# Performance work log

Measured on AMD Instinct MI355X. Metric: run time of the kernel, lower is better.

## Reference

```python
import jax, jax.numpy as jnp
import numpy as np

B, S, D, H, KD = 4, 2048, 640, 10, 64


def setup_inputs() -> dict:
    key = jax.random.key(0)
    k0, k1, k2, k3, k4 = jax.random.split(key, 5)
    x = jax.random.normal(k0, (B, S, D), dtype=jnp.float32)
    # per-head projection weights, stacked over heads: [H, D, KD]
    Wq = jax.random.normal(k1, (H, D, KD), dtype=jnp.float32) * 0.05
    Wk = jax.random.normal(k2, (H, D, KD), dtype=jnp.float32) * 0.05
    Wv = jax.random.normal(k3, (H, D, KD), dtype=jnp.float32) * 0.05
    # output projection: [H*KD, D]
    Wo = jax.random.normal(k4, (H * KD, D), dtype=jnp.float32) * 0.05
    return {"x": x, "Wq": Wq, "Wk": Wk, "Wv": Wv, "Wo": Wo}


def reference(x, Wq, Wk, Wv, Wo):
    # Batched equivalent of the per-head Python loop:
    # each head computes q=x@Wq_h, k=x@Wk_h, v=x@Wv_h, softmax(q k^T / sqrt(KD)) @ v
    q = jnp.einsum("bsd,hdk->bhsk", x, Wq)
    k = jnp.einsum("bsd,hdk->bhsk", x, Wk)
    v = jnp.einsum("bsd,hdk->bhsk", x, Wv)
    scale = 1.0 / jnp.sqrt(jnp.asarray(KD, x.dtype))
    scores = jnp.einsum("bhsk,bhtk->bhst", q, k) * scale  # [B,H,S,S]
    attn = jax.nn.softmax(scores, axis=-1)
    z = jnp.einsum("bhst,bhtk->bhsk", attn, v)  # [B,H,S,KD]
    # concat heads along last axis (head 0 first, matching the loop order)
    z = z.transpose(0, 2, 1, 3).reshape(x.shape[0], x.shape[1], H * KD)
    return jnp.einsum("bsf,fd->bsd", z, Wo)
```

## Files before the change

kernel.cpp:

```cpp
#include <hip/hip_runtime.h>
#include <hip/hip_bf16.h>

#define B_  4
#define S_  2048
#define D_  640
#define H_  10
#define KD_ 64

typedef __attribute__((ext_vector_type(8))) short  short8;
typedef __attribute__((ext_vector_type(4))) short  short4v;
typedef __attribute__((ext_vector_type(4))) float  floatx4;

static __device__ __forceinline__ short f2bf(float f) {
    union { __hip_bfloat16 h; short s; } u;
    u.h = __float2bfloat16(f);
    return u.s;
}

static __device__ __forceinline__ void gload_lds16(const void* gp, void* lp) {
    __builtin_amdgcn_global_load_lds(
        (const __attribute__((address_space(1))) unsigned int*)gp,
        (__attribute__((address_space(3))) unsigned int*)lp, 16, 0, 0);
}

__global__ __launch_bounds__(256) void pack_x(
        const float* __restrict__ x, short* __restrict__ xb) {
    int idx = (blockIdx.x * 256 + threadIdx.x) * 4;
    float4 v = *(const float4*)(x + idx);
    short4v o;
    o[0] = f2bf(v.x); o[1] = f2bf(v.y); o[2] = f2bf(v.z); o[3] = f2bf(v.w);
    *(short4v*)(xb + idx) = o;
}

__global__ __launch_bounds__(256) void transpose_w(
        const float* __restrict__ Wq, const float* __restrict__ Wk,
        const float* __restrict__ Wv, short* __restrict__ BigT) {
    __shared__ float tile[32][33];
    int m = blockIdx.z;
    int w = m / 10, h = m % 10;
    const float* W = ((w == 0) ? Wq : (w == 1) ? Wk : Wv) + h * 640 * 64;
    short* out = BigT + (w * 640 + h * 64) * 640;
    int c0 = blockIdx.x * 32;
    int r0 = blockIdx.y * 32;
    int tx = threadIdx.x & 31, ty = threadIdx.x >> 5;
    #pragma unroll
    for (int k = 0; k < 4; ++k)
        tile[ty + 8 * k][tx] = W[(r0 + ty + 8 * k) * 64 + c0 + tx];
    __syncthreads();
    #pragma unroll
    for (int k = 0; k < 4; ++k)
        out[(c0 + ty + 8 * k) * 640 + r0 + tx] = f2bf(tile[tx][ty + 8 * k]);
}

__global__ __launch_bounds__(256) void transpose_wo(
        const float* __restrict__ Wo, short* __restrict__ WoT) {
    __shared__ float tile[32][33];
    int c0 = blockIdx.x * 32;
    int r0 = blockIdx.y * 32;
    int tx = threadIdx.x & 31, ty = threadIdx.x >> 5;
    #pragma unroll
    for (int k = 0; k < 4; ++k)
        tile[ty + 8 * k][tx] = Wo[(r0 + ty + 8 * k) * 640 + c0 + tx];
    __syncthreads();
    #pragma unroll
    for (int k = 0; k < 4; ++k)
        WoT[(c0 + ty + 8 * k) * 640 + r0 + tx] = f2bf(tile[tx][ty + 8 * k]);
}

__global__ __launch_bounds__(256) void qkv_gemm(
        const short* __restrict__ X, const short* __restrict__ BigT,
        short* __restrict__ qb, short* __restrict__ kb, short* __restrict__ vtb) {
    __shared__ __align__(16) short Ab[128][64];
    __shared__ __align__(16) short Bb[128][64];

    int wave = threadIdx.x >> 6;
    int lane = threadIdx.x & 63;
    int lq = lane & 15, quad = lane >> 4;
    int wm = (wave & 1) * 64, wn = (wave >> 1) * 64;
    int tm = blockIdx.x * 128;
    int tn = blockIdx.y * 128;

    int r8 = lane >> 3;
    int sc = ((lane & 7) ^ r8) * 8;
    const short* Asrc = X    + (tm + wave * 32 + r8) * 640 + sc;
    const short* Bsrc = BigT + (tn + wave * 32 + r8) * 640 + sc;

    floatx4 acc[4][4];
    for (int a = 0; a < 4; ++a)
        for (int n = 0; n < 4; ++n)
            acc[a][n] = (floatx4){0.f, 0.f, 0.f, 0.f};

    int swz = lq & 7;
    for (int k0 = 0; k0 < 640; k0 += 64) {
        __syncthreads();
        #pragma unroll
        for (int c = 0; c < 4; ++c) {
            gload_lds16(Asrc + c * 8 * 640 + k0, &Ab[wave * 32 + c * 8][0]);
            gload_lds16(Bsrc + c * 8 * 640 + k0, &Bb[wave * 32 + c * 8][0]);
        }
        __syncthreads();

        #pragma unroll
        for (int ks = 0; ks < 2; ++ks) {
            short8 af[4], bf[4];
            #pragma unroll
            for (int t = 0; t < 4; ++t) {
                af[t] = *(const short8*)(&Ab[wm + t * 16 + lq][((ks * 4 + quad) ^ swz) * 8]);
                bf[t] = *(const short8*)(&Bb[wn + t * 16 + lq][((ks * 4 + quad) ^ swz) * 8]);
            }
            #pragma unroll
            for (int mt = 0; mt < 4; ++mt)
                #pragma unroll
                for (int nt = 0; nt < 4; ++nt)
                    acc[mt][nt] = __builtin_amdgcn_mfma_f32_16x16x32_bf16(
                        af[mt], bf[nt], acc[mt][nt], 0, 0, 0);
        }
    }

    const float qscale = 0.18033688011112042f;
    #pragma unroll
    for (int nt = 0; nt < 4; ++nt) {
        int n_base = tn + wn + nt * 16;
        int w = n_base / 640, rem = n_base % 640;
        int hh = rem / 64, kd = (rem % 64) + lq;
        #pragma unroll
        for (int mt = 0; mt < 4; ++mt) {
            #pragma unroll
            for (int r = 0; r < 4; ++r) {
                int m = tm + wm + mt * 16 + quad * 4 + r;
                int b = m >> 11, s = m & 2047;
                float val = acc[mt][nt][r];
                if (w == 0) {
                    qb[((b * H_ + hh) * S_ + s) * KD_ + kd] = f2bf(val * qscale);
                } else if (w == 1) {
                    kb[((b * H_ + hh) * S_ + s) * KD_ + kd] = f2bf(val);
                } else {
                    vtb[((b * H_ + hh) * KD_ + kd) * S_ + s] = f2bf(val);
                }
            }
        }
    }
}

__global__ __launch_bounds__(256) void attn(
        const short* __restrict__ qb, const short* __restrict__ kb,
        const short* __restrict__ vtb, short* __restrict__ zb) {
    __shared__ __align__(16) short Kbuf[2][64][64];
    __shared__ __align__(16) short Vbuf[2][64][64];
    __shared__ __align__(16) short Pbuf[4][16][72];

    int wave = threadIdx.x >> 6;
    int lane = threadIdx.x & 63;
    int lq = lane & 15, quad = lane >> 4;

    int bx = blockIdx.x;
    int xcd = bx & 7, slot = bx >> 3;
    int bh = xcd * 5 + (slot >> 5);
    int qt = slot & 31;
    int b = bh / 10, h = bh % 10;
    int q0 = qt * 64;

    const short* qp = qb + (b * H_ + h) * S_ * KD_;
    const short* kp = kb + (b * H_ + h) * S_ * KD_;
    const short* vp = vtb + (b * H_ + h) * KD_ * S_;

    int r8 = lane >> 3;
    int g  = (lane & 7) ^ r8;
    const short* kg0 = kp + (wave * 16 + r8) * 64 + g * 8;
    const short* kg1 = kp + (wave * 16 + 8 + r8) * 64 + g * 8;
    const short* vg0 = vp + (wave * 16 + r8) * (long)S_ + g * 8;
    const short* vg1 = vp + (wave * 16 + 8 + r8) * (long)S_ + g * 8;

    short8 qf0, qf1;
    {
        int row = q0 + wave * 16 + lq;
        qf0 = *(const short8*)(qp + row * 64 + quad * 8);
        qf1 = *(const short8*)(qp + row * 64 + 32 + quad * 8);
    }

    floatx4 O[4];
    for (int n = 0; n < 4; ++n) O[n] = (floatx4){0.f, 0.f, 0.f, 0.f};
    float lsum[4] = {0.f, 0.f, 0.f, 0.f};

    gload_lds16(kg0, &Kbuf[0][wave * 16][0]);
    gload_lds16(kg1, &Kbuf[0][wave * 16 + 8][0]);
    gload_lds16(vg0, &Vbuf[0][wave * 16][0]);
    gload_lds16(vg1, &Vbuf[0][wave * 16 + 8][0]);

    int p = 0;
    int sw = lq & 7;

    for (int t0 = 0; t0 < S_; t0 += 64) {
        __syncthreads();

        if (t0 + 64 < S_) {
            int pn = p ^ 1;
            gload_lds16(kg0 + (t0 + 64) * 64, &Kbuf[pn][wave * 16][0]);
            gload_lds16(kg1 + (t0 + 64) * 64, &Kbuf[pn][wave * 16 + 8][0]);
            gload_lds16(vg0 + (t0 + 64),      &Vbuf[pn][wave * 16][0]);
            gload_lds16(vg1 + (t0 + 64),      &Vbuf[pn][wave * 16 + 8][0]);
        }

        const short* Kb = &Kbuf[p][0][0];
        const short* Vb = &Vbuf[p][0][0];

        floatx4 sf[4];
        #pragma unroll
        for (int nt = 0; nt < 4; ++nt) {
            const short* krow = Kb + (nt * 16 + lq) * 64;
            short8 bk0 = *(const short8*)(krow + (quad ^ sw) * 8);
            short8 bk1 = *(const short8*)(krow + ((quad + 4) ^ sw) * 8);
            floatx4 z4 = (floatx4){0.f, 0.f, 0.f, 0.f};
            z4 = __builtin_amdgcn_mfma_f32_16x16x32_bf16(qf0, bk0, z4, 0, 0, 0);
            sf[nt] = __builtin_amdgcn_mfma_f32_16x16x32_bf16(qf1, bk1, z4, 0, 0, 0);
        }

        #pragma unroll
        for (int nt = 0; nt < 4; ++nt) {
            #pragma unroll
            for (int r = 0; r < 4; ++r) {
                float pv = __builtin_amdgcn_exp2f(sf[nt][r]);
                lsum[r] += pv;
                Pbuf[wave][quad * 4 + r][nt * 16 + lq] = f2bf(pv);
            }
        }

        #pragma unroll
        for (int ks = 0; ks < 2; ++ks) {
            short8 pf = *(const short8*)(&Pbuf[wave][lq][ks * 32 + quad * 8]);
            #pragma unroll
            for (int nt = 0; nt < 4; ++nt) {
                const short* vrow = Vb + (nt * 16 + lq) * 64;
                short8 bv = *(const short8*)(vrow + ((ks * 4 + quad) ^ sw) * 8);
                O[nt] = __builtin_amdgcn_mfma_f32_16x16x32_bf16(pf, bv, O[nt], 0, 0, 0);
            }
        }

        p ^= 1;
    }

    #pragma unroll
    for (int r = 0; r < 4; ++r) {
        float s = lsum[r];
        s += __shfl_xor(s, 1);
        s += __shfl_xor(s, 2);
        s += __shfl_xor(s, 4);
        s += __shfl_xor(s, 8);
        lsum[r] = s;
    }
    for (int nt = 0; nt < 4; ++nt) {
        for (int r = 0; r < 4; ++r) {
            int s = q0 + wave * 16 + quad * 4 + r;
            float o = O[nt][r] / lsum[r];
            zb[(b * S_ + s) * 640 + h * 64 + nt * 16 + lq] = f2bf(o);
        }
    }
}

__global__ __launch_bounds__(256) void out_gemm(
        const short* __restrict__ Z, const short* __restrict__ WoT,
        float* __restrict__ out) {
    __shared__ __align__(16) short Ab[128][64];
    __shared__ __align__(16) short Bb[128][64];

    int wave = threadIdx.x >> 6;
    int lane = threadIdx.x & 63;
    int lq = lane & 15, quad = lane >> 4;
    int wm = (wave & 1) * 64, wn = (wave >> 1) * 64;
    int tm = blockIdx.x * 128;
    int tn = blockIdx.y * 128;

    int r8 = lane >> 3;
    int sc = ((lane & 7) ^ r8) * 8;
    const short* Asrc = Z   + (tm + wave * 32 + r8) * 640 + sc;
    const short* Bsrc = WoT + (tn + wave * 32 + r8) * 640 + sc;

    floatx4 acc[4][4];
    for (int a = 0; a < 4; ++a)
        for (int n = 0; n < 4; ++n)
            acc[a][n] = (floatx4){0.f, 0.f, 0.f, 0.f};

    int swz = lq & 7;
    for (int k0 = 0; k0 < 640; k0 += 64) {
        __syncthreads();
        #pragma unroll
        for (int c = 0; c < 4; ++c) {
            gload_lds16(Asrc + c * 8 * 640 + k0, &Ab[wave * 32 + c * 8][0]);
            gload_lds16(Bsrc + c * 8 * 640 + k0, &Bb[wave * 32 + c * 8][0]);
        }
        __syncthreads();

        #pragma unroll
        for (int ks = 0; ks < 2; ++ks) {
            short8 af[4], bf[4];
            #pragma unroll
            for (int t = 0; t < 4; ++t) {
                af[t] = *(const short8*)(&Ab[wm + t * 16 + lq][((ks * 4 + quad) ^ swz) * 8]);
                bf[t] = *(const short8*)(&Bb[wn + t * 16 + lq][((ks * 4 + quad) ^ swz) * 8]);
            }
            #pragma unroll
            for (int mt = 0; mt < 4; ++mt)
                #pragma unroll
                for (int nt = 0; nt < 4; ++nt)
                    acc[mt][nt] = __builtin_amdgcn_mfma_f32_16x16x32_bf16(
                        af[mt], bf[nt], acc[mt][nt], 0, 0, 0);
        }
    }

    #pragma unroll
    for (int mt = 0; mt < 4; ++mt) {
        #pragma unroll
        for (int nt = 0; nt < 4; ++nt) {
            #pragma unroll
            for (int r = 0; r < 4; ++r) {
                int m = tm + wm + mt * 16 + quad * 4 + r;
                out[m * 640 + tn + wn + nt * 16 + lq] = acc[mt][nt][r];
            }
        }
    }
}

extern "C" void kernel_launch(void* const* d_in, const int* in_sizes, int n_in,
                              void* d_out, int out_size, void* d_ws, size_t ws_size,
                              hipStream_t stream) {
    const float* x  = (const float*)d_in[0];
    const float* Wq = (const float*)d_in[1];
    const float* Wk = (const float*)d_in[2];
    const float* Wv = (const float*)d_in[3];
    const float* Wo = (const float*)d_in[4];
    float* out = (float*)d_out;

    char* ws = (char*)d_ws;
    short* BigT = (short*)(ws);
    short* WoT  = (short*)(ws + 2457600);
    short* xb   = (short*)(ws + 3276800);
    short* qb   = (short*)(ws + 13762560);
    short* kb   = (short*)(ws + 24248320);
    short* vtb  = (short*)(ws + 34734080);
    short* zb   = (short*)(ws + 45219840);

    pack_x<<<dim3(5120), dim3(256), 0, stream>>>(x, xb);
    transpose_w<<<dim3(2, 20, 30), dim3(256), 0, stream>>>(Wq, Wk, Wv, BigT);
    transpose_wo<<<dim3(20, 20), dim3(256), 0, stream>>>(Wo, WoT);
    qkv_gemm<<<dim3(64, 15), dim3(256), 0, stream>>>(xb, BigT, qb, kb, vtb);
    attn<<<dim3(1280), dim3(256), 0, stream>>>(qb, kb, vtb, zb);
    out_gemm<<<dim3(64, 5), dim3(256), 0, stream>>>(zb, WoT, out);
}
```

Measured before the change: 218.7 us.

## Double attention query tile per block and merge prep kernels into one launch

```diff
diff --git a/kernel.cpp b/kernel.cpp
--- a/kernel.cpp
+++ b/kernel.cpp
@@ -23,48 +23,50 @@
         (__attribute__((address_space(3))) unsigned int*)lp, 16, 0, 0);
 }
 
-__global__ __launch_bounds__(256) void pack_x(
-        const float* __restrict__ x, short* __restrict__ xb) {
-    int idx = (blockIdx.x * 256 + threadIdx.x) * 4;
-    float4 v = *(const float4*)(x + idx);
-    short4v o;
-    o[0] = f2bf(v.x); o[1] = f2bf(v.y); o[2] = f2bf(v.z); o[3] = f2bf(v.w);
-    *(short4v*)(xb + idx) = o;
-}
-
-__global__ __launch_bounds__(256) void transpose_w(
+__global__ __launch_bounds__(256) void prep(
+        const float* __restrict__ x,
         const float* __restrict__ Wq, const float* __restrict__ Wk,
-        const float* __restrict__ Wv, short* __restrict__ BigT) {
+        const float* __restrict__ Wv, const float* __restrict__ Wo,
+        short* __restrict__ xb, short* __restrict__ BigT,
+        short* __restrict__ WoT) {
     __shared__ float tile[32][33];
-    int m = blockIdx.z;
-    int w = m / 10, h = m % 10;
-    const float* W = ((w == 0) ? Wq : (w == 1) ? Wk : Wv) + h * 640 * 64;
-    short* out = BigT + (w * 640 + h * 64) * 640;
-    int c0 = blockIdx.x * 32;
-    int r0 = blockIdx.y * 32;
-    int tx = threadIdx.x & 31, ty = threadIdx.x >> 5;
-    #pragma unroll
-    for (int k = 0; k < 4; ++k)
-        tile[ty + 8 * k][tx] = W[(r0 + ty + 8 * k) * 64 + c0 + tx];
-    __syncthreads();
-    #pragma unroll
-    for (int k = 0; k < 4; ++k)
-        out[(c0 + ty + 8 * k) * 640 + r0 + tx] = f2bf(tile[tx][ty + 8 * k]);
-}
-
-__global__ __launch_bounds__(256) void transpose_wo(
-        const float* __restrict__ Wo, short* __restrict__ WoT) {
-    __shared__ float tile[32][33];
-    int c0 = blockIdx.x * 32;
-    int r0 = blockIdx.y * 32;
-    int tx = threadIdx.x & 31, ty = threadIdx.x >> 5;
-    #pragma unroll
-    for (int k = 0; k < 4; ++k)
-        tile[ty + 8 * k][tx] = Wo[(r0 + ty + 8 * k) * 640 + c0 + tx];
-    __syncthreads();
-    #pragma unroll
-    for (int k = 0; k < 4; ++k)
-        WoT[(c0 + ty + 8 * k) * 640 + r0 + tx] = f2bf(tile[tx][ty + 8 * k]);
+    int bid = blockIdx.x;
+    if (bid < 5120) {
+        int idx = (bid * 256 + threadIdx.x) * 4;
+        float4 v = *(const float4*)(x + idx);
+        short4v o;
+        o[0] = f2bf(v.x); o[1] = f2bf(v.y); o[2] = f2bf(v.z); o[3] = f2bf(v.w);
+        *(short4v*)(xb + idx) = o;
+    } else if (bid < 6320) {
+        int flat = bid - 5120;
+        int bz = flat / 40, rem = flat % 40;
+        int by = rem >> 1, bxx = rem & 1;
+        int w = bz / 10, h = bz % 10;
+        const float* W = ((w == 0) ? Wq : (w == 1) ? Wk : Wv) + h * 640 * 64;
+        short* out = BigT + (w * 640 + h * 64) * 640;
+        int c0 = bxx * 32;
+        int r0 = by * 32;
+        int tx = threadIdx.x & 31, ty = threadIdx.x >> 5;
+        #pragma unroll
+        for (int k = 0; k < 4; ++k)
+            tile[ty + 8 * k][tx] = W[(r0 + ty + 8 * k) * 64 + c0 + tx];
+        __syncthreads();
+        #pragma unroll
+        for (int k = 0; k < 4; ++k)
+            out[(c0 + ty + 8 * k) * 640 + r0 + tx] = f2bf(tile[tx][ty + 8 * k]);
+    } else {
+        int flat = bid - 6320;
+        int c0 = (flat % 20) * 32;
+        int r0 = (flat / 20) * 32;
+        int tx = threadIdx.x & 31, ty = threadIdx.x >> 5;
+        #pragma unroll
+        for (int k = 0; k < 4; ++k)
+            tile[ty + 8 * k][tx] = Wo[(r0 + ty + 8 * k) * 640 + c0 + tx];
+        __syncthreads();
+        #pragma unroll
+        for (int k = 0; k < 4; ++k)
+            WoT[(c0 + ty + 8 * k) * 640 + r0 + tx] = f2bf(tile[tx][ty + 8 * k]);
+    }
 }
 
 __global__ __launch_bounds__(256) void qkv_gemm(
@@ -142,12 +144,12 @@
     }
 }
 
-__global__ __launch_bounds__(256) void attn(
+__global__ __launch_bounds__(256, 3) void attn(
         const short* __restrict__ qb, const short* __restrict__ kb,
         const short* __restrict__ vtb, short* __restrict__ zb) {
     __shared__ __align__(16) short Kbuf[2][64][64];
     __shared__ __align__(16) short Vbuf[2][64][64];
-    __shared__ __align__(16) short Pbuf[4][16][72];
+    __shared__ __align__(16) short Pbuf[4][2][16][72];
 
     int wave = threadIdx.x >> 6;
     int lane = threadIdx.x & 63;
@@ -155,10 +157,10 @@
 
     int bx = blockIdx.x;
     int xcd = bx & 7, slot = bx >> 3;
-    int bh = xcd * 5 + (slot >> 5);
-    int qt = slot & 31;
+    int bh = xcd * 5 + (slot >> 4);
+    int qt = slot & 15;
     int b = bh / 10, h = bh % 10;
-    int q0 = qt * 64;
+    int q0 = qt * 128;
 
     const short* qp = qb + (b * H_ + h) * S_ * KD_;
     const short* kp = kb + (b * H_ + h) * S_ * KD_;
@@ -171,16 +173,22 @@
     const short* vg0 = vp + (wave * 16 + r8) * (long)S_ + g * 8;
     const short* vg1 = vp + (wave * 16 + 8 + r8) * (long)S_ + g * 8;
 
-    short8 qf0, qf1;
+    short8 qA0, qA1, qB0, qB1;
     {
-        int row = q0 + wave * 16 + lq;
-        qf0 = *(const short8*)(qp + row * 64 + quad * 8);
-        qf1 = *(const short8*)(qp + row * 64 + 32 + quad * 8);
-    }
-
-    floatx4 O[4];
-    for (int n = 0; n < 4; ++n) O[n] = (floatx4){0.f, 0.f, 0.f, 0.f};
-    float lsum[4] = {0.f, 0.f, 0.f, 0.f};
+        int rowA = q0 + wave * 32 + lq;
+        qA0 = *(const short8*)(qp + rowA * 64 + quad * 8);
+        qA1 = *(const short8*)(qp + rowA * 64 + 32 + quad * 8);
+        qB0 = *(const short8*)(qp + (rowA + 16) * 64 + quad * 8);
+        qB1 = *(const short8*)(qp + (rowA + 16) * 64 + 32 + quad * 8);
+    }
+
+    floatx4 OA[4], OB[4];
+    for (int n = 0; n < 4; ++n) {
+        OA[n] = (floatx4){0.f, 0.f, 0.f, 0.f};
+        OB[n] = (floatx4){0.f, 0.f, 0.f, 0.f};
+    }
+    float lsumA[4] = {0.f, 0.f, 0.f, 0.f};
+    float lsumB[4] = {0.f, 0.f, 0.f, 0.f};
 
     gload_lds16(kg0, &Kbuf[0][wave * 16][0]);
     gload_lds16(kg1, &Kbuf[0][wave * 16 + 8][0]);
@@ -204,35 +212,43 @@
         const short* Kb = &Kbuf[p][0][0];
         const short* Vb = &Vbuf[p][0][0];
 
-        floatx4 sf[4];
+        floatx4 sA[4], sB[4];
         #pragma unroll
         for (int nt = 0; nt < 4; ++nt) {
             const short* krow = Kb + (nt * 16 + lq) * 64;
             short8 bk0 = *(const short8*)(krow + (quad ^ sw) * 8);
             short8 bk1 = *(const short8*)(krow + ((quad + 4) ^ sw) * 8);
-            floatx4 z4 = (floatx4){0.f, 0.f, 0.f, 0.f};
-            z4 = __builtin_amdgcn_mfma_f32_16x16x32_bf16(qf0, bk0, z4, 0, 0, 0);
-            sf[nt] = __builtin_amdgcn_mfma_f32_16x16x32_bf16(qf1, bk1, z4, 0, 0, 0);
+            floatx4 zA = (floatx4){0.f, 0.f, 0.f, 0.f};
+            zA = __builtin_amdgcn_mfma_f32_16x16x32_bf16(qA0, bk0, zA, 0, 0, 0);
+            sA[nt] = __builtin_amdgcn_mfma_f32_16x16x32_bf16(qA1, bk1, zA, 0, 0, 0);
+            floatx4 zB = (floatx4){0.f, 0.f, 0.f, 0.f};
+            zB = __builtin_amdgcn_mfma_f32_16x16x32_bf16(qB0, bk0, zB, 0, 0, 0);
+            sB[nt] = __builtin_amdgcn_mfma_f32_16x16x32_bf16(qB1, bk1, zB, 0, 0, 0);
         }
 
         #pragma unroll
         for (int nt = 0; nt < 4; ++nt) {
             #pragma unroll
             for (int r = 0; r < 4; ++r) {
-                float pv = __builtin_amdgcn_exp2f(sf[nt][r]);
-                lsum[r] += pv;
-                Pbuf[wave][quad * 4 + r][nt * 16 + lq] = f2bf(pv);
+                float pA = __builtin_amdgcn_exp2f(sA[nt][r]);
+                lsumA[r] += pA;
+                Pbuf[wave][0][quad * 4 + r][nt * 16 + lq] = f2bf(pA);
+                float pB = __builtin_amdgcn_exp2f(sB[nt][r]);
+                lsumB[r] += pB;
+                Pbuf[wave][1][quad * 4 + r][nt * 16 + lq] = f2bf(pB);
             }
         }
 
         #pragma unroll
         for (int ks = 0; ks < 2; ++ks) {
-            short8 pf = *(const short8*)(&Pbuf[wave][lq][ks * 32 + quad * 8]);
+            short8 pfA = *(const short8*)(&Pbuf[wave][0][lq][ks * 32 + quad * 8]);
+            short8 pfB = *(const short8*)(&Pbuf[wave][1][lq][ks * 32 + quad * 8]);
             #pragma unroll
             for (int nt = 0; nt < 4; ++nt) {
                 const short* vrow = Vb + (nt * 16 + lq) * 64;
                 short8 bv = *(const short8*)(vrow + ((ks * 4 + quad) ^ sw) * 8);
-                O[nt] = __builtin_amdgcn_mfma_f32_16x16x32_bf16(pf, bv, O[nt], 0, 0, 0);
+                OA[nt] = __builtin_amdgcn_mfma_f32_16x16x32_bf16(pfA, bv, OA[nt], 0, 0, 0);
+                OB[nt] = __builtin_amdgcn_mfma_f32_16x16x32_bf16(pfB, bv, OB[nt], 0, 0, 0);
             }
         }
 
@@ -241,18 +257,25 @@
 
     #pragma unroll
     for (int r = 0; r < 4; ++r) {
-        float s = lsum[r];
-        s += __shfl_xor(s, 1);
-        s += __shfl_xor(s, 2);
-        s += __shfl_xor(s, 4);
-        s += __shfl_xor(s, 8);
-        lsum[r] = s;
+        float sA2 = lsumA[r];
+        sA2 += __shfl_xor(sA2, 1);
+        sA2 += __shfl_xor(sA2, 2);
+        sA2 += __shfl_xor(sA2, 4);
+        sA2 += __shfl_xor(sA2, 8);
+        lsumA[r] = sA2;
+        float sB2 = lsumB[r];
+        sB2 += __shfl_xor(sB2, 1);
+        sB2 += __shfl_xor(sB2, 2);
+        sB2 += __shfl_xor(sB2, 4);
+        sB2 += __shfl_xor(sB2, 8);
+        lsumB[r] = sB2;
     }
     for (int nt = 0; nt < 4; ++nt) {
         for (int r = 0; r < 4; ++r) {
-            int s = q0 + wave * 16 + quad * 4 + r;
-            float o = O[nt][r] / lsum[r];
-            zb[(b * S_ + s) * 640 + h * 64 + nt * 16 + lq] = f2bf(o);
+            int sA3 = q0 + wave * 32 + quad * 4 + r;
+            zb[(b * S_ + sA3) * 640 + h * 64 + nt * 16 + lq] = f2bf(OA[nt][r] / lsumA[r]);
+            int sB3 = sA3 + 16;
+            zb[(b * S_ + sB3) * 640 + h * 64 + nt * 16 + lq] = f2bf(OB[nt][r] / lsumB[r]);
         }
     }
 }
@@ -339,10 +362,8 @@
     short* vtb  = (short*)(ws + 34734080);
     short* zb   = (short*)(ws + 45219840);
 
-    pack_x<<<dim3(5120), dim3(256), 0, stream>>>(x, xb);
-    transpose_w<<<dim3(2, 20, 30), dim3(256), 0, stream>>>(Wq, Wk, Wv, BigT);
-    transpose_wo<<<dim3(20, 20), dim3(256), 0, stream>>>(Wo, WoT);
+    prep<<<dim3(6720), dim3(256), 0, stream>>>(x, Wq, Wk, Wv, Wo, xb, BigT, WoT);
     qkv_gemm<<<dim3(64, 15), dim3(256), 0, stream>>>(xb, BigT, qb, kb, vtb);
-    attn<<<dim3(1280), dim3(256), 0, stream>>>(qb, kb, vtb, zb);
+    attn<<<dim3(640), dim3(256), 0, stream>>>(qb, kb, vtb, zb);
     out_gemm<<<dim3(64, 5), dim3(256), 0, stream>>>(zb, WoT, out);
 }
```

Result: faster. 206.3 us (-5.7%).
